# Kernel tuning notes

Hardware: AMD Instinct MI355X
Metric: run time of the kernel (lower is better)

## Reference

```python
import jax, jax.numpy as jnp
import numpy as np
from jax import lax

SLOPE = 0.01  # nn.LeakyReLU default negative slope

def leaky(x):
    return jnp.where(x >= 0, x, SLOPE * x)

def conv2d(x, w, b, pad):
    # x: [N,C,H,W], w: [O,I,kh,kw]
    y = lax.conv_general_dilated(x, w, (1, 1), [(pad, pad), (pad, pad)],
                                 dimension_numbers=('NCHW', 'OIHW', 'NCHW'))
    return y + b[None, :, None, None]

def centered_ifftn(x, axes):
    # np.fft.fftshift(np.fft.ifftn(np.fft.ifftshift(X), norm='ortho'))
    return jnp.fft.fftshift(jnp.fft.ifftn(jnp.fft.ifftshift(x, axes=axes), axes=axes, norm='ortho'), axes=axes)

def setup_inputs() -> dict:
    key = jax.random.key(0)
    ks = jax.random.split(key, 10)
    B, H, W, CK = 8, 640, 368, 32
    return {
        'img':    jax.random.normal(ks[0], (B, 1, H, W), jnp.float32),
        'kspace': jax.random.normal(ks[1], (B, 2, H, W), jnp.float32),
        # k_model1: Conv2d(2, CK, 3, padding=1) + LeakyReLU
        'wk': jax.random.normal(ks[2], (CK, 2, 3, 3), jnp.float32) * 0.1,
        'bk': jnp.zeros((CK,), jnp.float32),
        # conv1: Conv2d(CK, 2, kernel_size=1)
        'w1': jax.random.normal(ks[3], (2, CK, 1, 1), jnp.float32) * 0.1,
        'b1': jnp.zeros((2,), jnp.float32),
        # conv2: Conv2d(2, 1, kernel_size=1)
        'w2': jax.random.normal(ks[4], (1, 2, 1, 1), jnp.float32) * 0.1,
        'b2': jnp.zeros((1,), jnp.float32),
        # i_model1: Conv2d(1, 1, 3, padding=1) + LeakyReLU
        'wi': jax.random.normal(ks[5], (1, 1, 3, 3), jnp.float32) * 0.1,
        'bi': jnp.zeros((1,), jnp.float32),
    }

def reference(img, kspace, wk, bk, w1, b1, w2, b2, wi, bi):
    # k-space branch: k_model1 then conv1 + LeakyReLU
    out1 = leaky(conv2d(leaky(conv2d(kspace, wk, bk, 1)), w1, b1, 0))  # [B,2,H,W]
    # channel 0 = real, channel 1 = imag; ifftn over ALL axes (incl. batch),
    # exactly as the original numpy call with axes=range(out.ndim)
    cplx = out1[:, 0].astype(jnp.complex64) + 1j * out1[:, 1].astype(jnp.complex64)  # [B,H,W]
    im = jnp.abs(centered_ifftn(cplx, (0, 1, 2)))[:, None]  # [B,1,H,W]
    # concat with image, cast to half (torch.cuda.HalfTensor), conv2 + LeakyReLU
    out = jnp.concatenate([im, img], axis=1).astype(jnp.float16)  # [B,2,H,W]
    out = leaky(conv2d(out, w2.astype(jnp.float16), b2.astype(jnp.float16), 0))
    out = out.astype(jnp.float32)  # [B,1,H,W]
    # image-domain model
    return leaky(conv2d(out, wi, bi, 1))  # [B,1,H,W]
```

## Files before the change

### kernel.cpp

```cpp
#include <hip/hip_runtime.h>
#include <hip/hip_fp16.h>
#include <math.h>

#define B_ 8
#define H_ 640
#define W_ 368
#define HW_ (H_*W_)
#define NP_ (B_*H_*W_)

#define FROWS 4
#define HLINES 4
#define TS 16

typedef __attribute__((ext_vector_type(8))) short v8s;
typedef __attribute__((ext_vector_type(16))) float v16f;

__device__ __forceinline__ float leaky_(float x){ return fmaxf(x, 0.01f*x); }

__device__ __forceinline__ unsigned short f2bf(float x){
    unsigned u = __float_as_uint(x);
    u += 0x7FFFu + ((u >> 16) & 1u);
    return (unsigned short)(u >> 16);
}

__device__ __forceinline__ float2 cadd_(float2 a, float2 b){ return make_float2(a.x+b.x, a.y+b.y); }
__device__ __forceinline__ float2 csub_(float2 a, float2 b){ return make_float2(a.x-b.x, a.y-b.y); }
__device__ __forceinline__ float2 cmul_(float2 a, float c, float s){
    return make_float2(a.x*c - a.y*s, a.x*s + a.y*c);
}
__device__ __forceinline__ float2 cmulv_(float2 a, float2 w){
    return make_float2(a.x*w.x - a.y*w.y, a.x*w.y + a.y*w.x);
}

__device__ __forceinline__ void dft4p_(float2 p0, float2 p1, float2 p2, float2 p3,
                                       float2& z0, float2& z1, float2& z2, float2& z3){
    float2 s0 = cadd_(p0,p2), d0 = csub_(p0,p2);
    float2 s1 = cadd_(p1,p3), d1 = csub_(p1,p3);
    z0 = cadd_(s0,s1);
    z2 = csub_(s0,s1);
    z1 = make_float2(d0.x - d1.y, d0.y + d1.x);
    z3 = make_float2(d0.x + d1.y, d0.y - d1.x);
}

__device__ __forceinline__ void fft16p_(const float2* x, float2* X){
    const float C1 = 0.9238795325112867f, S1 = 0.3826834323650898f;
    const float R  = 0.7071067811865476f;
    float2 Y[4][4];
    #pragma unroll
    for (int b = 0; b < 4; ++b)
        dft4p_(x[b], x[4+b], x[8+b], x[12+b], Y[b][0], Y[b][1], Y[b][2], Y[b][3]);
    Y[1][1] = cmul_(Y[1][1],  C1,  S1);
    Y[1][2] = cmul_(Y[1][2],   R,   R);
    Y[1][3] = cmul_(Y[1][3],  S1,  C1);
    Y[2][1] = cmul_(Y[2][1],   R,   R);
    Y[2][2] = make_float2(-Y[2][2].y, Y[2][2].x);
    Y[2][3] = cmul_(Y[2][3],  -R,   R);
    Y[3][1] = cmul_(Y[3][1],  S1,  C1);
    Y[3][2] = cmul_(Y[3][2],  -R,   R);
    Y[3][3] = cmul_(Y[3][3], -C1, -S1);
    #pragma unroll
    for (int c = 0; c < 4; ++c)
        dft4p_(Y[0][c], Y[1][c], Y[2][c], Y[3][c], X[c], X[c+4], X[c+8], X[c+12]);
}

__device__ __forceinline__ void fft8p_(const float2* x, float2* X){
    const float R = 0.7071067811865476f;
    float2 Y0[4], Y1[4];
    dft4p_(x[0], x[2], x[4], x[6], Y0[0], Y0[1], Y0[2], Y0[3]);
    dft4p_(x[1], x[3], x[5], x[7], Y1[0], Y1[1], Y1[2], Y1[3]);
    float2 T0 = Y1[0];
    float2 T1 = cmul_(Y1[1],  R, R);
    float2 T2 = make_float2(-Y1[2].y, Y1[2].x);
    float2 T3 = cmul_(Y1[3], -R, R);
    X[0] = cadd_(Y0[0], T0);  X[4] = csub_(Y0[0], T0);
    X[1] = cadd_(Y0[1], T1);  X[5] = csub_(Y0[1], T1);
    X[2] = cadd_(Y0[2], T2);  X[6] = csub_(Y0[2], T2);
    X[3] = cadd_(Y0[3], T3);  X[7] = csub_(Y0[3], T3);
}

__global__ void init_tables_kernel(float2* __restrict__ T){
    int i = blockIdx.x*blockDim.x + threadIdx.x;
    if (i >= 1301) return;
    int r, c, modN; int j;
    if      (i <  368){ j = i;        r = j%16; c = j/16; modN = 368; }
    else if (i < 1008){ j = i-368;    r = j%16; c = j/16; modN = 640; }
    else if (i < 1048){ j = i-1008;   r = j%8;  c = j/8;  modN = 40;  }
    else              { j = i-1048;   r = j/11; c = j%11 + 1; modN = 23; }
    int t = (int)(((long long)r * c) % modN);
    if (t > modN/2) t -= modN;
    float ang = (float)(6.283185307179586 * ((double)t / (double)modN));
    float s, co;
    sincosf(ang, &s, &co);
    T[i] = make_float2(co, s);
}

__global__ __launch_bounds__(256) void kfftw_kernel(const float* __restrict__ ksp,
                               const float* __restrict__ wk,
                               const float* __restrict__ bk,
                               const float* __restrict__ w1,
                               const float* __restrict__ b1,
                               const float2* __restrict__ TW368P,
                               const float2* __restrict__ F23P,
                               float2* __restrict__ Bt){
    __shared__ unsigned short Sb[4836];
    __shared__ float2 X[FROWS*369];
    int t = threadIdx.x;
    int blk = blockIdx.x;
    int b  = blk / 160;
    int h0 = (blk - b*160) * FROWS;

    for (int seg = 0; seg < 12; ++seg){
        int r = seg >> 1, ic = seg & 1;
        int hh = h0 - 1 + r;
        int ok = ((unsigned)hh < 640u);
        const float* base = ksp + ((size_t)(b*2 + ic)*640 + (ok ? hh : 0))*368;
        for (int col = t; col < 372; col += 256){
            int c = col - 1;
            float v = (ok && (unsigned)c < 368u) ? base[c] : 0.f;
            Sb[seg*372 + col] = f2bf(v);
        }
    }
    for (int i = t; i < 372; i += 256) Sb[4464 + i] = 0;

    int lane = t & 63, wave = t >> 6;
    int ch = lane & 31, h = lane >> 5;
    int l = wave;

    int offB[8];
    v8s a1, a2;
    #pragma unroll
    for (int j = 0; j < 8; ++j){
        int kk = 8*h + j;
        int ic = (kk >= 9) ? 1 : 0;
        int tt = kk - ic*9;
        int ty = tt/3, tx = tt - ty*3;
        offB[j] = ((ty + l)*2 + ic)*372 + tx;
        a1[j] = (short)f2bf(wk[ch*18 + kk]);
        a2[j] = 0;
    }
    if (h == 0){
        a2[0] = (short)f2bf(wk[ch*18 + 16]);
        a2[1] = (short)f2bf(wk[ch*18 + 17]);
        a2[2] = (short)f2bf(bk[ch]);
    }
    const int off16 = ((2 + l)*2 + 1)*372 + 1;
    const int off17 = off16 + 1;

    float wp0[16], wp1[16];
    #pragma unroll
    for (int r = 0; r < 16; ++r){
        int row = (r & 3) + 8*(r >> 2) + 4*h;
        wp0[r] = w1[row];
        wp1[r] = w1[32 + row];
    }
    float b10 = b1[0], b11 = b1[1];
    float sgn = (ch & 1) ? -1.f : 1.f;
    __syncthreads();

    for (int g = 0; g < 12; ++g){
        int px = g*32 + ch;
        v8s bv;
        #pragma unroll
        for (int j = 0; j < 8; ++j) bv[j] = (short)Sb[offB[j] + px];
        v16f d = {0.f,0.f,0.f,0.f,0.f,0.f,0.f,0.f,0.f,0.f,0.f,0.f,0.f,0.f,0.f,0.f};
        d = __builtin_amdgcn_mfma_f32_32x32x16_bf16(a1, bv, d, 0, 0, 0);
        v8s b2v = {0,0,0,0,0,0,0,0};
        b2v[0] = (short)Sb[off16 + px];
        b2v[1] = (short)Sb[off17 + px];
        b2v[2] = (short)0x3F80;
        d = __builtin_amdgcn_mfma_f32_32x32x16_bf16(a2, b2v, d, 0, 0, 0);
        float sx = 0.f, sy = 0.f;
        #pragma unroll
        for (int r = 0; r < 16; ++r){
            float y = leaky_(d[r]);
            sx = fmaf(y, wp0[r], sx);
            sy = fmaf(y, wp1[r], sy);
        }
        sx += __shfl_xor(sx, 32);
        sy += __shfl_xor(sy, 32);
        if (h == 0 && px < 368){
            float o0 = leaky_(sx + b10);
            float o1 = leaky_(sy + b11);
            X[l*369 + px] = make_float2(sgn*o0, sgn*o1);
        }
    }
    asm volatile("" ::: "memory");

    if (lane < 23){
        int n2 = lane;
        float2 xr[16], Xo[16];
        #pragma unroll
        for (int n1 = 0; n1 < 16; ++n1) xr[n1] = X[l*369 + 23*n1 + n2];
        fft16p_(xr, Xo);
        const float2* row = TW368P + n2*16;
        #pragma unroll
        for (int k1 = 0; k1 < 16; ++k1)
            X[l*369 + 23*k1 + n2] = cmulv_(Xo[k1], row[k1]);
    }
    asm volatile("" ::: "memory");

    {
        int k1 = lane & 15, qr = lane >> 4;
        const float2* xp = X + l*369 + 23*k1;
        float2 x0 = xp[0];
        float2 u[11], d[11];
        #pragma unroll
        for (int m = 1; m <= 11; ++m){
            float2 a = xp[m], bb = xp[23-m];
            u[m-1] = cadd_(a, bb);
            d[m-1] = csub_(a, bb);
        }
        asm volatile("" ::: "memory");
        int k2beg = qr*6;
        int k2end = (qr == 3) ? 23 : k2beg + 6;
        for (int k2 = k2beg; k2 < k2end; ++k2){
            const float2* row = F23P + k2*11;
            float re = x0.x, im = x0.y;
            #pragma unroll
            for (int m = 0; m < 11; ++m){
                float c = row[m].x, s = row[m].y;
                re += u[m].x*c - d[m].y*s;
                im += u[m].y*c + d[m].x*s;
            }
            X[l*369 + k1 + 16*k2] = make_float2(re, im);
        }
    }
    __syncthreads();

    const float sc = 0.052129458158616354f;
    for (int i = t; i < FROWS*368; i += 256){
        int k = i >> 2, ll = i & 3;
        float2 v = X[ll*369 + k];
        float s = (k & 1) ? -sc : sc;
        Bt[((size_t)(b*368 + k))*640 + h0 + ll] = make_float2(v.x*s, v.y*s);
    }
}

__global__ __launch_bounds__(256) void fftH_kernel(const float2* __restrict__ Bt,
                                                   const float2* __restrict__ TW640P,
                                                   const float2* __restrict__ TW40P,
                                                   float2* __restrict__ A2){
    __shared__ float2 X[HLINES][656];
    int t = threadIdx.x;
    int lane = t & 63, l = t >> 6;
    size_t lineb = (size_t)blockIdx.x * (HLINES*640) + (size_t)l*640;

    for (int n = lane; n < 640; n += 64){
        float2 v = Bt[lineb + n];
        float s = (n & 1) ? -1.f : 1.f;
        X[l][n + n/40] = make_float2(v.x*s, v.y*s);
    }
    asm volatile("" ::: "memory");

    if (lane < 40){
        int n2 = lane;
        float2 xr[16], Xo[16];
        #pragma unroll
        for (int n1 = 0; n1 < 16; ++n1) xr[n1] = X[l][41*n1 + n2];
        fft16p_(xr, Xo);
        const float2* row = TW640P + n2*16;
        #pragma unroll
        for (int k1 = 0; k1 < 16; ++k1)
            X[l][41*k1 + n2] = cmulv_(Xo[k1], row[k1]);
    }
    asm volatile("" ::: "memory");

    #pragma unroll
    for (int pass = 0; pass < 2; ++pass){
        int it = lane + pass*64;
        if (it < 80){
            int k1 = it & 15, m2 = it >> 4;
            float2 xr[8], Xo[8];
            #pragma unroll
            for (int m1 = 0; m1 < 8; ++m1) xr[m1] = X[l][41*k1 + 5*m1 + m2];
            fft8p_(xr, Xo);
            const float2* row = TW40P + m2*8;
            #pragma unroll
            for (int j1 = 0; j1 < 8; ++j1)
                X[l][41*k1 + 5*j1 + m2] = cmulv_(Xo[j1], row[j1]);
        }
    }
    asm volatile("" ::: "memory");

    {
        const float CK1[5] = {1.f,  0.30901699437494745f, -0.8090169943749475f, -0.8090169943749475f,  0.30901699437494745f};
        const float SK1[5] = {0.f,  0.9510565162951535f,   0.5877852522924731f, -0.5877852522924731f, -0.9510565162951535f};
        const float CK2[5] = {1.f, -0.8090169943749475f,   0.30901699437494745f, 0.30901699437494745f, -0.8090169943749475f};
        const float SK2[5] = {0.f,  0.5877852522924731f,  -0.9510565162951535f,  0.9510565162951535f, -0.5877852522924731f};
        int k10 = lane & 15, j10 = lane >> 4;
        int j11 = j10 + 4;
        float2 p0[5], p1[5];
        #pragma unroll
        for (int m2 = 0; m2 < 5; ++m2) p0[m2] = X[l][41*k10 + 5*j10 + m2];
        #pragma unroll
        for (int m2 = 0; m2 < 5; ++m2) p1[m2] = X[l][41*k10 + 5*j11 + m2];
        asm volatile("" ::: "memory");
        float2 u0a = cadd_(p0[1], p0[4]), d0a = csub_(p0[1], p0[4]);
        float2 u0b = cadd_(p0[2], p0[3]), d0b = csub_(p0[2], p0[3]);
        float2 u1a = cadd_(p1[1], p1[4]), d1a = csub_(p1[1], p1[4]);
        float2 u1b = cadd_(p1[2], p1[3]), d1b = csub_(p1[2], p1[3]);
        #pragma unroll
        for (int j2 = 0; j2 < 5; ++j2){
            float c1v = CK1[j2], s1v = SK1[j2], c2v = CK2[j2], s2v = SK2[j2];
            float re0 = p0[0].x + u0a.x*c1v - d0a.y*s1v + u0b.x*c2v - d0b.y*s2v;
            float im0 = p0[0].y + u0a.y*c1v + d0a.x*s1v + u0b.y*c2v + d0b.x*s2v;
            float re1 = p1[0].x + u1a.x*c1v - d1a.y*s1v + u1b.x*c2v - d1b.y*s2v;
            float im1 = p1[0].y + u1a.y*c1v + d1a.x*s1v + u1b.y*c2v + d1b.x*s2v;
            int ka = k10 + 16*j10 + 128*j2;
            int kb = k10 + 16*j11 + 128*j2;
            X[l][ka + ka/40] = make_float2(re0, im0);
            X[l][kb + kb/40] = make_float2(re1, im1);
        }
    }
    asm volatile("" ::: "memory");

    const float sc = 0.03952847075210474f;
    for (int k = lane; k < 640; k += 64){
        float2 v = X[l][k + k/40];
        float s = (k & 1) ? -sc : sc;
        A2[lineb + k] = make_float2(v.x*s, v.y*s);
    }
}

__global__ __launch_bounds__(256) void tail_kernel(const float2* __restrict__ A2,
                                  const float* __restrict__ img,
                                  const float* __restrict__ w2,
                                  const float* __restrict__ b2,
                                  const float* __restrict__ wi,
                                  const float* __restrict__ bi,
                                  float* __restrict__ out){
    __shared__ float Pl[8][TS+2][TS+3];
    int t = threadIdx.x;
    int ty0 = (blockIdx.x / 23) * TS;
    int tx0 = (blockIdx.x % 23) * TS;

    float w2h0 = __half2float(__float2half(w2[0]));
    float w2h1 = __half2float(__float2half(w2[1]));
    float b2h  = __half2float(__float2half(b2[0]));
    const float sc8 = 0.35355339059327373f;

    for (int idx = t; idx < (TS+2)*(TS+2); idx += 256){
        int hx = idx / (TS+2), hy = idx - hx*(TS+2);
        int hh = ty0 - 1 + hy, ww = tx0 - 1 + hx;
        int hc = min(max(hh, 0), H_-1), wc = min(max(ww, 0), W_-1);
        float2 x[8], Xo[8];
        #pragma unroll
        for (int n = 0; n < 8; ++n){
            float2 v = A2[((size_t)(n*368 + wc))*640 + hc];
            float s = (n & 1) ? -1.f : 1.f;
            x[n] = make_float2(v.x*s, v.y*s);
        }
        fft8p_(x, Xo);
        #pragma unroll
        for (int k = 0; k < 8; ++k){
            float s = (k & 1) ? -sc8 : sc8;
            float yr = Xo[k].x * s, yi = Xo[k].y * s;
            float mag = sqrtf(yr*yr + yi*yi);
            Pl[k][hy][hx] = __half2float(__float2half(mag));
        }
    }
    __syncthreads();

    for (int idx = t; idx < (TS+2)*(TS+2); idx += 256){
        int hy = idx / (TS+2), hx = idx - hy*(TS+2);
        int hh = ty0 - 1 + hy, ww = tx0 - 1 + hx;
        bool inb = (hh >= 0) && (hh < H_) && (ww >= 0) && (ww < W_);
        int hc = min(max(hh, 0), H_-1), wc = min(max(ww, 0), W_-1);
        float inbf = inb ? 1.f : 0.f;
        #pragma unroll
        for (int k = 0; k < 8; ++k){
            float g = __half2float(__float2half(img[(size_t)k*HW_ + hc*W_ + wc]));
            float a = Pl[k][hy][hx];
            float o = leaky_(a*w2h0 + g*w2h1 + b2h);
            o = __half2float(__float2half(o));
            Pl[k][hy][hx] = o * inbf;
        }
    }
    __syncthreads();

    int sy = t >> 4, sx = t & 15;
    float wv[9];
    #pragma unroll
    for (int q = 0; q < 9; ++q) wv[q] = wi[q];
    float bi0 = bi[0];
    #pragma unroll
    for (int k = 0; k < 8; ++k){
        float acc = bi0;
        #pragma unroll
        for (int dy = 0; dy < 3; ++dy)
            #pragma unroll
            for (int dx = 0; dx < 3; ++dx)
                acc += wv[dy*3+dx] * Pl[k][sy+dy][sx+dx];
        out[((size_t)k*H_ + ty0+sy)*W_ + tx0+sx] = leaky_(acc);
    }
}

extern "C" void kernel_launch(void* const* d_in, const int* in_sizes, int n_in,
                              void* d_out, int out_size, void* d_ws, size_t ws_size,
                              hipStream_t stream){
    const float* img = (const float*)d_in[0];
    const float* ksp = (const float*)d_in[1];
    const float* wk  = (const float*)d_in[2];
    const float* bk  = (const float*)d_in[3];
    const float* w1  = (const float*)d_in[4];
    const float* b1  = (const float*)d_in[5];
    const float* w2  = (const float*)d_in[6];
    const float* b2  = (const float*)d_in[7];
    const float* wi  = (const float*)d_in[8];
    const float* bi  = (const float*)d_in[9];

    char* ws = (char*)d_ws;
    float2* Bt  = (float2*)(ws + 0);
    float2* A2  = (float2*)(ws + 15073280);
    float2* T   = (float2*)(ws + 30146560);
    float2* TW368P = T + 0;
    float2* TW640P = T + 368;
    float2* TW40P  = T + 1008;
    float2* F23P   = T + 1048;
    float* out  = (float*)d_out;

    init_tables_kernel<<<6, 256, 0, stream>>>(T);

    kfftw_kernel<<<B_*(H_/FROWS), 256, 0, stream>>>(ksp, wk, bk, w1, b1,
                                                    TW368P, F23P, Bt);
    fftH_kernel<<<(B_*W_)/HLINES, 256, 0, stream>>>(Bt, TW640P, TW40P, A2);
    tail_kernel<<<(H_/TS)*(W_/TS), 256, 0, stream>>>(A2, img, w2, b2, wi, bi, out);
}
```

Measured before the change: 156.9 us.

## Fuse batch-axis FFT and magnitude into H-FFT kernel, store half magnitudes

```diff
diff --git a/kernel.cpp b/kernel.cpp
--- a/kernel.cpp
+++ b/kernel.cpp
@@ -9,8 +9,8 @@
 #define NP_ (B_*H_*W_)
 
 #define FROWS 4
-#define HLINES 4
-#define TS 16
+#define TH 64
+#define TWI 8
 
 typedef __attribute__((ext_vector_type(8))) short v8s;
 typedef __attribute__((ext_vector_type(16))) float v16f;
@@ -236,14 +236,15 @@
     }
 }
 
-__global__ __launch_bounds__(256) void fftH_kernel(const float2* __restrict__ Bt,
-                                                   const float2* __restrict__ TW640P,
-                                                   const float2* __restrict__ TW40P,
-                                                   float2* __restrict__ A2){
-    __shared__ float2 X[HLINES][656];
+__global__ __launch_bounds__(512) void fftHB_kernel(const float2* __restrict__ Bt,
+                                                    const float2* __restrict__ TW640P,
+                                                    const float2* __restrict__ TW40P,
+                                                    __half* __restrict__ M){
+    __shared__ float2 X[B_][656];
     int t = threadIdx.x;
     int lane = t & 63, l = t >> 6;
-    size_t lineb = (size_t)blockIdx.x * (HLINES*640) + (size_t)l*640;
+    int w = blockIdx.x;
+    size_t lineb = ((size_t)l*W_ + w)*640;
 
     for (int n = lane; n < 640; n += 64){
         float2 v = Bt[lineb + n];
@@ -312,86 +313,92 @@
             X[l][kb + kb/40] = make_float2(re1, im1);
         }
     }
-    asm volatile("" ::: "memory");
-
-    const float sc = 0.03952847075210474f;
-    for (int k = lane; k < 640; k += 64){
-        float2 v = X[l][k + k/40];
-        float s = (k & 1) ? -sc : sc;
-        A2[lineb + k] = make_float2(v.x*s, v.y*s);
-    }
-}
-
-__global__ __launch_bounds__(256) void tail_kernel(const float2* __restrict__ A2,
+    __syncthreads();
+
+    const float sc640 = 0.03952847075210474f;
+    const float sc8   = 0.35355339059327373f;
+    for (int hh = t; hh < 640; hh += 512){
+        int p = hh + hh/40;
+        float sh = (hh & 1) ? -sc640 : sc640;
+        float2 x[8], Xo[8];
+        #pragma unroll
+        for (int n = 0; n < 8; ++n){
+            float2 v = X[n][p];
+            float s = (n & 1) ? -sh : sh;
+            x[n] = make_float2(v.x*s, v.y*s);
+        }
+        fft8p_(x, Xo);
+        #pragma unroll
+        for (int k = 0; k < 8; ++k){
+            float s = (k & 1) ? -sc8 : sc8;
+            float yr = Xo[k].x * s, yi = Xo[k].y * s;
+            float mag = sqrtf(yr*yr + yi*yi);
+            M[((size_t)k*W_ + w)*640 + hh] = __float2half(mag);
+        }
+    }
+}
+
+__global__ __launch_bounds__(256) void tail2_kernel(const __half* __restrict__ M,
                                   const float* __restrict__ img,
                                   const float* __restrict__ w2,
                                   const float* __restrict__ b2,
                                   const float* __restrict__ wi,
                                   const float* __restrict__ bi,
                                   float* __restrict__ out){
-    __shared__ float Pl[8][TS+2][TS+3];
+    __shared__ float Pl[B_][TWI+2][TH+4];
+    __shared__ float Pc[B_][TH+2][TWI+4];
     int t = threadIdx.x;
-    int ty0 = (blockIdx.x / 23) * TS;
-    int tx0 = (blockIdx.x % 23) * TS;
+    int th0 = (blockIdx.x / 46) * TH;
+    int tw0 = (blockIdx.x % 46) * TWI;
 
     float w2h0 = __half2float(__float2half(w2[0]));
     float w2h1 = __half2float(__float2half(w2[1]));
     float b2h  = __half2float(__float2half(b2[0]));
-    const float sc8 = 0.35355339059327373f;
-
-    for (int idx = t; idx < (TS+2)*(TS+2); idx += 256){
-        int hx = idx / (TS+2), hy = idx - hx*(TS+2);
-        int hh = ty0 - 1 + hy, ww = tx0 - 1 + hx;
-        int hc = min(max(hh, 0), H_-1), wc = min(max(ww, 0), W_-1);
-        float2 x[8], Xo[8];
-        #pragma unroll
-        for (int n = 0; n < 8; ++n){
-            float2 v = A2[((size_t)(n*368 + wc))*640 + hc];
-            float s = (n & 1) ? -1.f : 1.f;
-            x[n] = make_float2(v.x*s, v.y*s);
-        }
-        fft8p_(x, Xo);
-        #pragma unroll
-        for (int k = 0; k < 8; ++k){
-            float s = (k & 1) ? -sc8 : sc8;
-            float yr = Xo[k].x * s, yi = Xo[k].y * s;
-            float mag = sqrtf(yr*yr + yi*yi);
-            Pl[k][hy][hx] = __half2float(__float2half(mag));
-        }
+
+    for (int idx = t; idx < B_*10*66; idx += 256){
+        int b = idx / 660; int r = idx - b*660;
+        int wr = r / 66, hh = r - wr*66;
+        int wg = tw0 - 1 + wr, hg = th0 - 1 + hh;
+        float m = 0.f;
+        if ((unsigned)wg < (unsigned)W_ && (unsigned)hg < (unsigned)H_)
+            m = __half2float(M[((size_t)b*W_ + wg)*640 + hg]);
+        Pl[b][wr][hh] = m;
     }
     __syncthreads();
 
-    for (int idx = t; idx < (TS+2)*(TS+2); idx += 256){
-        int hy = idx / (TS+2), hx = idx - hy*(TS+2);
-        int hh = ty0 - 1 + hy, ww = tx0 - 1 + hx;
-        bool inb = (hh >= 0) && (hh < H_) && (ww >= 0) && (ww < W_);
-        int hc = min(max(hh, 0), H_-1), wc = min(max(ww, 0), W_-1);
-        float inbf = inb ? 1.f : 0.f;
-        #pragma unroll
-        for (int k = 0; k < 8; ++k){
-            float g = __half2float(__float2half(img[(size_t)k*HW_ + hc*W_ + wc]));
-            float a = Pl[k][hy][hx];
-            float o = leaky_(a*w2h0 + g*w2h1 + b2h);
-            o = __half2float(__float2half(o));
-            Pl[k][hy][hx] = o * inbf;
-        }
+    for (int idx = t; idx < B_*66*10; idx += 256){
+        int b = idx / 660; int r = idx - b*660;
+        int hh = r / 10, wr = r - hh*10;
+        int wg = tw0 - 1 + wr, hg = th0 - 1 + hh;
+        float p = 0.f;
+        if ((unsigned)wg < (unsigned)W_ && (unsigned)hg < (unsigned)H_){
+            float g = __half2float(__float2half(img[((size_t)b*H_ + hg)*W_ + wg]));
+            float m = Pl[b][wr][hh];
+            float o = leaky_(m*w2h0 + g*w2h1 + b2h);
+            p = __half2float(__float2half(o));
+        }
+        Pc[b][hh][wr] = p;
     }
     __syncthreads();
 
-    int sy = t >> 4, sx = t & 15;
+    int sw = t & 7, sh_ = t >> 3;
     float wv[9];
     #pragma unroll
     for (int q = 0; q < 9; ++q) wv[q] = wi[q];
     float bi0 = bi[0];
     #pragma unroll
-    for (int k = 0; k < 8; ++k){
-        float acc = bi0;
-        #pragma unroll
-        for (int dy = 0; dy < 3; ++dy)
+    for (int b = 0; b < B_; ++b){
+        #pragma unroll
+        for (int hb = 0; hb < 2; ++hb){
+            int hl = sh_ + 32*hb;
+            float acc = bi0;
             #pragma unroll
-            for (int dx = 0; dx < 3; ++dx)
-                acc += wv[dy*3+dx] * Pl[k][sy+dy][sx+dx];
-        out[((size_t)k*H_ + ty0+sy)*W_ + tx0+sx] = leaky_(acc);
+            for (int dy = 0; dy < 3; ++dy)
+                #pragma unroll
+                for (int dx = 0; dx < 3; ++dx)
+                    acc += wv[dy*3+dx] * Pc[b][hl+dy][sw+dx];
+            out[((size_t)b*H_ + th0+hl)*W_ + tw0+sw] = leaky_(acc);
+        }
     }
 }
 
@@ -411,7 +418,7 @@
 
     char* ws = (char*)d_ws;
     float2* Bt  = (float2*)(ws + 0);
-    float2* A2  = (float2*)(ws + 15073280);
+    __half* M   = (__half*)(ws + 15073280);
     float2* T   = (float2*)(ws + 30146560);
     float2* TW368P = T + 0;
     float2* TW640P = T + 368;
@@ -423,6 +430,6 @@
 
     kfftw_kernel<<<B_*(H_/FROWS), 256, 0, stream>>>(ksp, wk, bk, w1, b1,
                                                     TW368P, F23P, Bt);
-    fftH_kernel<<<(B_*W_)/HLINES, 256, 0, stream>>>(Bt, TW640P, TW40P, A2);
-    tail_kernel<<<(H_/TS)*(W_/TS), 256, 0, stream>>>(A2, img, w2, b2, wi, bi, out);
-}
+    fftHB_kernel<<<W_, 512, 0, stream>>>(Bt, TW640P, TW40P, M);
+    tail2_kernel<<<(H_/TH)*(W_/TWI), 256, 0, stream>>>(M, img, w2, b2, wi, bi, out);
+}
```

Measured after the change: 161.5 us. +3.0%, slower.

## Restructure tail into column-wave conv with shuffles; one line per fftH block

Applied to the files above, without the earlier changes.

```diff
diff --git a/kernel.cpp b/kernel.cpp
--- a/kernel.cpp
+++ b/kernel.cpp
@@ -9,8 +9,6 @@
 #define NP_ (B_*H_*W_)
 
 #define FROWS 4
-#define HLINES 4
-#define TS 16
 
 typedef __attribute__((ext_vector_type(8))) short v8s;
 typedef __attribute__((ext_vector_type(16))) float v16f;
@@ -22,6 +20,8 @@
     u += 0x7FFFu + ((u >> 16) & 1u);
     return (unsigned short)(u >> 16);
 }
+
+__device__ __forceinline__ float hrnd_(float x){ return __half2float(__float2half(x)); }
 
 __device__ __forceinline__ float2 cadd_(float2 a, float2 b){ return make_float2(a.x+b.x, a.y+b.y); }
 __device__ __forceinline__ float2 csub_(float2 a, float2 b){ return make_float2(a.x-b.x, a.y-b.y); }
@@ -236,19 +236,18 @@
     }
 }
 
-__global__ __launch_bounds__(256) void fftH_kernel(const float2* __restrict__ Bt,
-                                                   const float2* __restrict__ TW640P,
-                                                   const float2* __restrict__ TW40P,
-                                                   float2* __restrict__ A2){
-    __shared__ float2 X[HLINES][656];
-    int t = threadIdx.x;
-    int lane = t & 63, l = t >> 6;
-    size_t lineb = (size_t)blockIdx.x * (HLINES*640) + (size_t)l*640;
+__global__ __launch_bounds__(64) void fftH_kernel(const float2* __restrict__ Bt,
+                                                  const float2* __restrict__ TW640P,
+                                                  const float2* __restrict__ TW40P,
+                                                  float2* __restrict__ A2){
+    __shared__ float2 X[656];
+    int lane = threadIdx.x;
+    size_t lineb = (size_t)blockIdx.x * 640;
 
     for (int n = lane; n < 640; n += 64){
         float2 v = Bt[lineb + n];
         float s = (n & 1) ? -1.f : 1.f;
-        X[l][n + n/40] = make_float2(v.x*s, v.y*s);
+        X[n + n/40] = make_float2(v.x*s, v.y*s);
     }
     asm volatile("" ::: "memory");
 
@@ -256,12 +255,12 @@
         int n2 = lane;
         float2 xr[16], Xo[16];
         #pragma unroll
-        for (int n1 = 0; n1 < 16; ++n1) xr[n1] = X[l][41*n1 + n2];
+        for (int n1 = 0; n1 < 16; ++n1) xr[n1] = X[41*n1 + n2];
         fft16p_(xr, Xo);
         const float2* row = TW640P + n2*16;
         #pragma unroll
         for (int k1 = 0; k1 < 16; ++k1)
-            X[l][41*k1 + n2] = cmulv_(Xo[k1], row[k1]);
+            X[41*k1 + n2] = cmulv_(Xo[k1], row[k1]);
     }
     asm volatile("" ::: "memory");
 
@@ -272,12 +271,12 @@
             int k1 = it & 15, m2 = it >> 4;
             float2 xr[8], Xo[8];
             #pragma unroll
-            for (int m1 = 0; m1 < 8; ++m1) xr[m1] = X[l][41*k1 + 5*m1 + m2];
+            for (int m1 = 0; m1 < 8; ++m1) xr[m1] = X[41*k1 + 5*m1 + m2];
             fft8p_(xr, Xo);
             const float2* row = TW40P + m2*8;
             #pragma unroll
             for (int j1 = 0; j1 < 8; ++j1)
-                X[l][41*k1 + 5*j1 + m2] = cmulv_(Xo[j1], row[j1]);
+                X[41*k1 + 5*j1 + m2] = cmulv_(Xo[j1], row[j1]);
         }
     }
     asm volatile("" ::: "memory");
@@ -291,9 +290,9 @@
         int j11 = j10 + 4;
         float2 p0[5], p1[5];
         #pragma unroll
-        for (int m2 = 0; m2 < 5; ++m2) p0[m2] = X[l][41*k10 + 5*j10 + m2];
-        #pragma unroll
-        for (int m2 = 0; m2 < 5; ++m2) p1[m2] = X[l][41*k10 + 5*j11 + m2];
+        for (int m2 = 0; m2 < 5; ++m2) p0[m2] = X[41*k10 + 5*j10 + m2];
+        #pragma unroll
+        for (int m2 = 0; m2 < 5; ++m2) p1[m2] = X[41*k10 + 5*j11 + m2];
         asm volatile("" ::: "memory");
         float2 u0a = cadd_(p0[1], p0[4]), d0a = csub_(p0[1], p0[4]);
         float2 u0b = cadd_(p0[2], p0[3]), d0b = csub_(p0[2], p0[3]);
@@ -308,90 +307,92 @@
             float im1 = p1[0].y + u1a.y*c1v + d1a.x*s1v + u1b.y*c2v + d1b.x*s2v;
             int ka = k10 + 16*j10 + 128*j2;
             int kb = k10 + 16*j11 + 128*j2;
-            X[l][ka + ka/40] = make_float2(re0, im0);
-            X[l][kb + kb/40] = make_float2(re1, im1);
+            X[ka + ka/40] = make_float2(re0, im0);
+            X[kb + kb/40] = make_float2(re1, im1);
         }
     }
     asm volatile("" ::: "memory");
 
     const float sc = 0.03952847075210474f;
     for (int k = lane; k < 640; k += 64){
-        float2 v = X[l][k + k/40];
+        float2 v = X[k + k/40];
         float s = (k & 1) ? -sc : sc;
         A2[lineb + k] = make_float2(v.x*s, v.y*s);
     }
 }
 
-__global__ __launch_bounds__(256) void tail_kernel(const float2* __restrict__ A2,
+__global__ __launch_bounds__(256) void tail3_kernel(const float2* __restrict__ A2,
                                   const float* __restrict__ img,
                                   const float* __restrict__ w2,
                                   const float* __restrict__ b2,
                                   const float* __restrict__ wi,
                                   const float* __restrict__ bi,
                                   float* __restrict__ out){
-    __shared__ float Pl[8][TS+2][TS+3];
+    __shared__ float Ot[B_][62][5];
     int t = threadIdx.x;
-    int ty0 = (blockIdx.x / 23) * TS;
-    int tx0 = (blockIdx.x % 23) * TS;
-
-    float w2h0 = __half2float(__float2half(w2[0]));
-    float w2h1 = __half2float(__float2half(w2[1]));
-    float b2h  = __half2float(__float2half(b2[0]));
+    int lane = t & 63, wv = t >> 6;
+    int wtile = blockIdx.x % 92;
+    int htile = blockIdx.x / 92;
+    int w  = wtile*4 + wv;
+    int h0 = htile*62;
+    int hg = h0 - 1 + lane;
+    int hc = min(max(hg, 0), H_-1);
+    bool hok = ((unsigned)hg < (unsigned)H_);
+
+    float w2h0 = hrnd_(w2[0]);
+    float w2h1 = hrnd_(w2[1]);
+    float b2h  = hrnd_(b2[0]);
     const float sc8 = 0.35355339059327373f;
 
-    for (int idx = t; idx < (TS+2)*(TS+2); idx += 256){
-        int hx = idx / (TS+2), hy = idx - hx*(TS+2);
-        int hh = ty0 - 1 + hy, ww = tx0 - 1 + hx;
-        int hc = min(max(hh, 0), H_-1), wc = min(max(ww, 0), W_-1);
+    float p[B_][3];
+    #pragma unroll
+    for (int dw = 0; dw < 3; ++dw){
+        int wq = w - 1 + dw;
+        bool wok = ((unsigned)wq < (unsigned)W_);
+        int wc = min(max(wq, 0), W_-1);
         float2 x[8], Xo[8];
         #pragma unroll
         for (int n = 0; n < 8; ++n){
-            float2 v = A2[((size_t)(n*368 + wc))*640 + hc];
+            float2 v = A2[((size_t)(n*W_ + wc))*640 + hc];
             float s = (n & 1) ? -1.f : 1.f;
             x[n] = make_float2(v.x*s, v.y*s);
         }
         fft8p_(x, Xo);
+        float msk = (wok && hok) ? 1.f : 0.f;
         #pragma unroll
         for (int k = 0; k < 8; ++k){
             float s = (k & 1) ? -sc8 : sc8;
             float yr = Xo[k].x * s, yi = Xo[k].y * s;
-            float mag = sqrtf(yr*yr + yi*yi);
-            Pl[k][hy][hx] = __half2float(__float2half(mag));
-        }
+            float mag = hrnd_(sqrtf(yr*yr + yi*yi));
+            float g = hrnd_(img[((size_t)k*H_ + hc)*W_ + wc]);
+            float o = hrnd_(leaky_(mag*w2h0 + g*w2h1 + b2h));
+            p[k][dw] = o * msk;
+        }
+    }
+
+    float wv9[9];
+    #pragma unroll
+    for (int q = 0; q < 9; ++q) wv9[q] = wi[q];
+    float bi0 = bi[0];
+    #pragma unroll
+    for (int b = 0; b < B_; ++b){
+        float s0 = fmaf(wv9[0], p[b][0], fmaf(wv9[1], p[b][1], wv9[2]*p[b][2]));
+        float s1 = fmaf(wv9[3], p[b][0], fmaf(wv9[4], p[b][1], wv9[5]*p[b][2]));
+        float s2 = fmaf(wv9[6], p[b][0], fmaf(wv9[7], p[b][1], wv9[8]*p[b][2]));
+        float up = __shfl_up(s0, 1);
+        float dn = __shfl_down(s2, 1);
+        float acc = bi0 + up + s1 + dn;
+        if (lane >= 1 && lane <= 62 && hg < H_)
+            Ot[b][lane-1][wv] = leaky_(acc);
     }
     __syncthreads();
 
-    for (int idx = t; idx < (TS+2)*(TS+2); idx += 256){
-        int hy = idx / (TS+2), hx = idx - hy*(TS+2);
-        int hh = ty0 - 1 + hy, ww = tx0 - 1 + hx;
-        bool inb = (hh >= 0) && (hh < H_) && (ww >= 0) && (ww < W_);
-        int hc = min(max(hh, 0), H_-1), wc = min(max(ww, 0), W_-1);
-        float inbf = inb ? 1.f : 0.f;
-        #pragma unroll
-        for (int k = 0; k < 8; ++k){
-            float g = __half2float(__float2half(img[(size_t)k*HW_ + hc*W_ + wc]));
-            float a = Pl[k][hy][hx];
-            float o = leaky_(a*w2h0 + g*w2h1 + b2h);
-            o = __half2float(__float2half(o));
-            Pl[k][hy][hx] = o * inbf;
-        }
-    }
-    __syncthreads();
-
-    int sy = t >> 4, sx = t & 15;
-    float wv[9];
-    #pragma unroll
-    for (int q = 0; q < 9; ++q) wv[q] = wi[q];
-    float bi0 = bi[0];
-    #pragma unroll
-    for (int k = 0; k < 8; ++k){
-        float acc = bi0;
-        #pragma unroll
-        for (int dy = 0; dy < 3; ++dy)
-            #pragma unroll
-            for (int dx = 0; dx < 3; ++dx)
-                acc += wv[dy*3+dx] * Pl[k][sy+dy][sx+dx];
-        out[((size_t)k*H_ + ty0+sy)*W_ + tx0+sx] = leaky_(acc);
+    for (int idx = t; idx < B_*62*4; idx += 256){
+        int b = idx / 248; int r = idx - b*248;
+        int hl = r >> 2, wq = r & 3;
+        int hh = h0 + hl;
+        if (hh < H_)
+            out[((size_t)b*H_ + hh)*W_ + wtile*4 + wq] = Ot[b][hl][wq];
     }
 }
 
@@ -423,6 +424,6 @@
 
     kfftw_kernel<<<B_*(H_/FROWS), 256, 0, stream>>>(ksp, wk, bk, w1, b1,
                                                     TW368P, F23P, Bt);
-    fftH_kernel<<<(B_*W_)/HLINES, 256, 0, stream>>>(Bt, TW640P, TW40P, A2);
-    tail_kernel<<<(H_/TS)*(W_/TS), 256, 0, stream>>>(A2, img, w2, b2, wi, bi, out);
-}
+    fftH_kernel<<<B_*W_, 64, 0, stream>>>(Bt, TW640P, TW40P, A2);
+    tail3_kernel<<<92*11, 256, 0, stream>>>(A2, img, w2, b2, wi, bi, out);
+}
```

Measured after the change: 174.3 us. 11.1% more time.
